# Kernel optimization log

Hardware: AMD Instinct MI355X
Metric: run time of the kernel (lower is better)

The kernel has to match this reference:

```python
import jax, jax.numpy as jnp
import numpy as np

N_HEADS = 16
ROPE_THETA = 10000.0


def _rotate_half(x):
    d = x.shape[-1] // 2
    return jnp.concatenate([-x[..., d:], x[..., :d]], axis=-1)


def setup_inputs() -> dict:
    key = jax.random.key(0)
    k1, k2, k3, k4 = jax.random.split(key, 4)
    B, S, D = 2, 2048, 2048
    std = 0.02
    return {
        "x": jax.random.normal(k1, (B, S, D), dtype=jnp.float32),
        "wq": std * jax.random.normal(k2, (D, D), dtype=jnp.float32),
        "wkv": std * jax.random.normal(k3, (D, 2 * D), dtype=jnp.float32),
        "wo": std * jax.random.normal(k4, (D, D), dtype=jnp.float32),
    }


def reference(x, wq, wkv, wo):
    # prefill case: kv_cache=None, past_length=0
    B, S, D = x.shape
    H = N_HEADS
    dh = D // H

    Q = x @ wq.T                                   # [B,S,D]
    K, V = jnp.split(x @ wkv, 2, axis=-1)          # [B,S,D] each

    q = Q.reshape(B, S, H, dh).transpose(0, 2, 1, 3)  # [B,H,S,dh]
    k = K.reshape(B, S, H, dh).transpose(0, 2, 1, 3)
    v = V.reshape(B, S, H, dh).transpose(0, 2, 1, 3)

    # RoPE tables (cos/sin of outer(pos, inv_freq), duplicated across halves)
    inv_freq = 1.0 / (ROPE_THETA ** (jnp.arange(0, dh, 2, dtype=jnp.float32) / dh))
    emb = jnp.arange(S, dtype=jnp.float32)[:, None] * inv_freq[None, :]  # [S, dh/2]
    cos = jnp.tile(jnp.cos(emb), (1, 2))[None, None]  # [1,1,S,dh]
    sin = jnp.tile(jnp.sin(emb), (1, 2))[None, None]

    q = q * cos + _rotate_half(q) * sin
    k = k * cos + _rotate_half(k) * sin

    scale = 1.0 / jnp.sqrt(jnp.asarray(dh, dtype=x.dtype))
    scores = jnp.einsum('bhqd,bhkd->bhqk', q, k) * scale  # [B,H,S,S]
    causal = jnp.tril(jnp.ones((S, S), dtype=bool))
    scores = jnp.where(causal[None, None], scores, -jnp.inf)
    attn = jax.nn.softmax(scores, axis=-1)

    out = jnp.einsum('bhqk,bhkd->bhqd', attn, v)          # [B,H,S,dh]
    out = out.transpose(0, 2, 1, 3).reshape(B, S, D)
    return out @ wo.T
```

## Files before the change

kernel.cpp:

```cpp
#include <hip/hip_runtime.h>
#include <stdint.h>

typedef unsigned short u16;
typedef __attribute__((ext_vector_type(8))) short short8;
typedef __attribute__((ext_vector_type(4))) float floatx4;

#define MFMA16(a, b, c) __builtin_amdgcn_mfma_f32_16x16x32_bf16(a, b, c, 0, 0, 0)

static __device__ __forceinline__ void gl_lds16(const void* g, void* l) {
  __builtin_amdgcn_global_load_lds(
      (const __attribute__((address_space(1))) uint32_t*)g,
      (__attribute__((address_space(3))) uint32_t*)l, 16, 0, 0);
}

static __device__ __forceinline__ float b2f(u16 u) {
  union { float f; unsigned u; } v;
  v.u = ((unsigned)u) << 16;
  return v.f;
}
static __device__ __forceinline__ u16 f2b(float f) {
  union { float f; unsigned u; } v;
  v.f = f;
  unsigned r = v.u + 0x7fffu + ((v.u >> 16) & 1u);
  return (u16)(r >> 16);
}
static __device__ __forceinline__ u16 f2b_rn(float f) {
  union { float f; unsigned u; } v;
  v.f = f;
  return (u16)((v.u + 0x8000u) >> 16);
}

static __device__ __forceinline__ int is_f32(const int* __restrict__ flag) {
  int s = 0;
#pragma unroll
  for (int i = 0; i < 32; ++i) s += flag[i];
  return s > 1000;
}

template <int CTRL>
static __device__ __forceinline__ float dppf(float x) {
  return __builtin_bit_cast(
      float, __builtin_amdgcn_update_dpp(0, __builtin_bit_cast(int, x), CTRL,
                                         0xF, 0xF, true));
}
static __device__ __forceinline__ float sum16(float x) {
  x += dppf<0x128>(x);
  x += dppf<0x124>(x);
  x += dppf<0x122>(x);
  x += dppf<0x121>(x);
  return x;
}
static __device__ __forceinline__ float max16(float x) {
  x = fmaxf(x, dppf<0x128>(x));
  x = fmaxf(x, dppf<0x124>(x));
  x = fmaxf(x, dppf<0x122>(x));
  x = fmaxf(x, dppf<0x121>(x));
  return x;
}

__global__ __launch_bounds__(256) void detect_f32(const u16* __restrict__ x,
                                                  int* __restrict__ flag) {
  __shared__ int cnt[256];
  int i = blockIdx.x * 256 + threadIdx.x;
  short8 v = ((const short8*)x)[i];
  int c = 0;
#pragma unroll
  for (int j = 0; j < 8; ++j) {
    int e = (((unsigned short)v[j]) >> 7) & 0xFF;
    c += (e >= 140) ? 1 : 0;
  }
  cnt[threadIdx.x] = c;
  __syncthreads();
  for (int s = 128; s > 0; s >>= 1) {
    if (threadIdx.x < (unsigned)s) cnt[threadIdx.x] += cnt[threadIdx.x + s];
    __syncthreads();
  }
  if (threadIdx.x == 0) flag[blockIdx.x] = cnt[0];
}

static __device__ __forceinline__ void conv8_body(const void* __restrict__ src,
                                                  u16* __restrict__ dst, int i,
                                                  int f32) {
  short8 r;
  if (f32) {
    const float4* s = (const float4*)src;
    float4 a = s[2 * i], b = s[2 * i + 1];
    r[0] = (short)f2b(a.x); r[1] = (short)f2b(a.y);
    r[2] = (short)f2b(a.z); r[3] = (short)f2b(a.w);
    r[4] = (short)f2b(b.x); r[5] = (short)f2b(b.y);
    r[6] = (short)f2b(b.z); r[7] = (short)f2b(b.w);
  } else {
    r = ((const short8*)src)[i];
  }
  ((short8*)dst)[i] = r;
}

__global__ __launch_bounds__(256) void convert_in8(const void* __restrict__ src,
                                                   u16* __restrict__ dst, int n8,
                                                   const int* __restrict__ flag) {
  int i = blockIdx.x * 256 + threadIdx.x;
  if (i >= n8) return;
  conv8_body(src, dst, i, is_f32(flag));
}

__global__ __launch_bounds__(256) void prep_fused(const void* __restrict__ x,
                                                  const void* __restrict__ wq,
                                                  const void* __restrict__ wkv,
                                                  u16* __restrict__ xb,
                                                  u16* __restrict__ wqb,
                                                  u16* __restrict__ wkvT,
                                                  const int* __restrict__ flag) {
  __shared__ u16 tile[32][33];
  int bid = blockIdx.x;
  int f = is_f32(flag);
  if (bid < 4096) {
    conv8_body(x, xb, bid * 256 + threadIdx.x, f);
  } else if (bid < 6144) {
    conv8_body(wq, wqb, (bid - 4096) * 256 + threadIdx.x, f);
  } else {
    int tb = bid - 6144;
    int c0 = (tb & 127) * 32, r0 = (tb >> 7) * 32;
    int lx = threadIdx.x & 31, ly = threadIdx.x >> 5;
#pragma unroll
    for (int i = 0; i < 32; i += 8) {
      size_t idx = (size_t)(r0 + ly + i) * 4096 + c0 + lx;
      tile[ly + i][lx] = f ? f2b(((const float*)wkv)[idx]) : ((const u16*)wkv)[idx];
    }
    __syncthreads();
#pragma unroll
    for (int i = 0; i < 32; i += 8)
      wkvT[(size_t)(c0 + ly + i) * 2048 + r0 + lx] = tile[lx][ly + i];
  }
}

__global__ __launch_bounds__(256) void mid_fused(u16* __restrict__ KV,
                                                 u16* __restrict__ Vt,
                                                 u16* __restrict__ Q) {
  __shared__ u16 tile[32][33];
  int bid = blockIdx.x;
  if (bid < 8192) {
    int b = bid >> 12;
    int d0 = (bid & 63) * 32, s0 = ((bid >> 6) & 63) * 32;
    int lx = threadIdx.x & 31, ly = threadIdx.x >> 5;
    const u16* src = KV + ((size_t)(b * 2048 + s0)) * 4096 + 2048 + d0;
#pragma unroll
    for (int i = 0; i < 32; i += 8)
      tile[ly + i][lx] = src[(size_t)(ly + i) * 4096 + lx];
    __syncthreads();
    u16* dst = Vt + ((size_t)(b * 2048 + d0)) * 2048 + s0;
#pragma unroll
    for (int i = 0; i < 32; i += 8)
      dst[(size_t)(ly + i) * 2048 + lx] = tile[lx][ly + i];
  } else {
    const float scale = 0.08838834764831845f;
    int idx = (bid - 8192) * 256 + threadIdx.x;
    int tok = idx >> 10;
    int rem = idx & 1023;
    int h = rem >> 6, i = rem & 63;
    int pos = tok & 2047;
    float f = __powf(10000.0f, -(float)(2 * i) * (1.0f / 128.0f));
    float ang = (float)pos * f;
    float s, c;
    sincosf(ang, &s, &c);

    size_t qb = (size_t)tok * 2048 + h * 128 + i;
    float q1 = b2f(Q[qb]), q2 = b2f(Q[qb + 64]);
    Q[qb] = f2b((q1 * c - q2 * s) * scale);
    Q[qb + 64] = f2b((q2 * c + q1 * s) * scale);

    size_t kb = (size_t)tok * 4096 + h * 128 + i;
    float k1 = b2f(KV[kb]), k2 = b2f(KV[kb + 64]);
    KV[kb] = f2b(k1 * c - k2 * s);
    KV[kb + 64] = f2b(k2 * c + k1 * s);
  }
}

__global__ __launch_bounds__(256) void gemm_nt(const u16* __restrict__ A,
                                               const u16* __restrict__ Bm,
                                               void* __restrict__ Cv,
                                               int M, int N, int K,
                                               const int* __restrict__ flag,
                                               int flag_mode) {
  __shared__ u16 Ash[128 * 64];
  __shared__ u16 Bsh[128 * 64];
  int tid = threadIdx.x, w = tid >> 6, lane = tid & 63;
  int quad = lane >> 4, l15 = lane & 15;
  int m0 = blockIdx.y * 128, n0 = blockIdx.x * 128;
  int wm = (w & 1) * 64, wn = (w >> 1) * 64;
  int f32out = flag_mode ? is_f32(flag) : 0;

  floatx4 acc[4][4];
#pragma unroll
  for (int i = 0; i < 4; ++i)
#pragma unroll
    for (int j = 0; j < 4; ++j) acc[i][j] = floatx4{0.f, 0.f, 0.f, 0.f};

  int srow = lane >> 3;
  int gch = (lane & 7) ^ srow;
  const u16* Ag = A + (size_t)(m0 + w * 32 + srow) * K + gch * 8;
  const u16* Bg = Bm + (size_t)(n0 + w * 32 + srow) * K + gch * 8;

  for (int k0 = 0; k0 < K; k0 += 64) {
    __syncthreads();
#pragma unroll
    for (int t = 0; t < 4; ++t) {
      gl_lds16(Ag + (size_t)t * 8 * K + k0, (void*)(Ash + (w * 32 + t * 8) * 64));
      gl_lds16(Bg + (size_t)t * 8 * K + k0, (void*)(Bsh + (w * 32 + t * 8) * 64));
    }
    __syncthreads();
#pragma unroll
    for (int kk = 0; kk < 2; ++kk) {
      int c = kk * 4 + quad;
      short8 af[4], bf[4];
#pragma unroll
      for (int i = 0; i < 4; ++i) {
        int m = wm + 16 * i + l15;
        af[i] = *(const short8*)(Ash + m * 64 + ((c ^ (m & 7)) << 3));
        int n = wn + 16 * i + l15;
        bf[i] = *(const short8*)(Bsh + n * 64 + ((c ^ (n & 7)) << 3));
      }
#pragma unroll
      for (int i = 0; i < 4; ++i)
#pragma unroll
        for (int j = 0; j < 4; ++j) acc[i][j] = MFMA16(af[i], bf[j], acc[i][j]);
    }
  }

#pragma unroll
  for (int i = 0; i < 4; ++i)
#pragma unroll
    for (int r = 0; r < 4; ++r) {
      int row = m0 + wm + 16 * i + quad * 4 + r;
      if (f32out) {
        float* cp = (float*)Cv + (size_t)row * N + n0 + wn + l15;
#pragma unroll
        for (int j = 0; j < 4; ++j) cp[16 * j] = acc[i][j][r];
      } else {
        u16* cp = (u16*)Cv + (size_t)row * N + n0 + wn + l15;
#pragma unroll
        for (int j = 0; j < 4; ++j) cp[16 * j] = f2b(acc[i][j][r]);
      }
    }
}

__global__ __launch_bounds__(512, 2) void gemm8(const u16* __restrict__ A,
                                                const u16* __restrict__ Bm,
                                                void* __restrict__ Cv,
                                                int M, int N, int K,
                                                const int* __restrict__ flag,
                                                int flag_mode) {
  __shared__ u16 Ash[2 * 256 * 64];
  __shared__ u16 Bsh[2 * 256 * 64];
  int tid = threadIdx.x, w = tid >> 6, lane = tid & 63;
  int quad = lane >> 4, l15 = lane & 15;
  int wr = w >> 2, wc = w & 3;
  int wm = wr * 128, wn = wc * 64;
  int m0 = blockIdx.y * 256, n0 = blockIdx.x * 256;
  int f32out = flag_mode ? is_f32(flag) : 0;
  const int NT = K >> 6;

  int srow8 = lane >> 3;
  int gch = (lane & 7) ^ srow8;
  const u16* Ag = A + (size_t)(m0 + w * 8 + srow8) * K + gch * 8;
  const u16* Bg = Bm + (size_t)(n0 + w * 8 + srow8) * K + gch * 8;
  int ldsrow = w * 8;

  floatx4 acc[8][4];
#pragma unroll
  for (int i = 0; i < 8; ++i)
#pragma unroll
    for (int j = 0; j < 4; ++j) acc[i][j] = floatx4{0.f, 0.f, 0.f, 0.f};

  int ch0 = ((quad ^ (l15 & 7)) << 3);
  int ch1 = (((4 + quad) ^ (l15 & 7)) << 3);

  auto stage = [&](int qi) {
    int tau = qi >> 2;
    int tc = tau < NT ? tau : NT - 1;
    int hh = qi & 3;
    int half = (hh & 1) * 128;
    int sbuf = (tau & 1) * (256 * 64);
    size_t kof = (size_t)tc * 64;
    if (hh < 2) {
      gl_lds16(Bg + (size_t)half * K + kof,
               (void*)(Bsh + sbuf + (half + ldsrow) * 64));
      gl_lds16(Bg + (size_t)(half + 64) * K + kof,
               (void*)(Bsh + sbuf + (half + 64 + ldsrow) * 64));
    } else {
      gl_lds16(Ag + (size_t)half * K + kof,
               (void*)(Ash + sbuf + (half + ldsrow) * 64));
      gl_lds16(Ag + (size_t)(half + 64) * K + kof,
               (void*)(Ash + sbuf + (half + 64 + ldsrow) * 64));
    }
  };

  stage(0); stage(1); stage(2); stage(3);
  __asm__ volatile("s_waitcnt vmcnt(4)" ::: "memory");
  stage(4); stage(5); stage(6);
  __asm__ volatile("s_waitcnt vmcnt(6)" ::: "memory");
  __builtin_amdgcn_s_barrier();

  for (int t = 0; t < NT; ++t) {
    u16* As = Ash + (t & 1) * (256 * 64);
    u16* Bs = Bsh + (t & 1) * (256 * 64);
    if (t) {
      __asm__ volatile("s_waitcnt vmcnt(6)" ::: "memory");
      __builtin_amdgcn_s_barrier();
    }
    int qb = 7 + 4 * t;
    short8 bf[8], af0[8], af1[8];

#pragma unroll
    for (int j = 0; j < 4; ++j) {
      int n = wn + 16 * j + l15;
      bf[2 * j] = *(const short8*)(Bs + n * 64 + ch0);
    }
#pragma unroll
    for (int i = 0; i < 4; ++i) {
      int m = wm + 16 * i + l15;
      af0[2 * i] = *(const short8*)(As + m * 64 + ch0);
    }
    stage(qb);
    __builtin_amdgcn_s_barrier();
    __asm__ volatile("s_waitcnt lgkmcnt(0)" ::: "memory");
    __builtin_amdgcn_sched_barrier(0);
    __builtin_amdgcn_s_setprio(1);
#pragma unroll
    for (int i = 0; i < 4; ++i)
#pragma unroll
      for (int j = 0; j < 4; ++j)
        acc[i][j] = MFMA16(af0[2 * i], bf[2 * j], acc[i][j]);
    __builtin_amdgcn_s_setprio(0);
    __builtin_amdgcn_s_barrier();

#pragma unroll
    for (int j = 0; j < 4; ++j) {
      int n = wn + 16 * j + l15;
      bf[2 * j + 1] = *(const short8*)(Bs + n * 64 + ch1);
    }
#pragma unroll
    for (int i = 0; i < 4; ++i) {
      int m = wm + 16 * i + l15;
      af0[2 * i + 1] = *(const short8*)(As + m * 64 + ch1);
    }
    stage(qb + 1);
    __builtin_amdgcn_s_barrier();
    __asm__ volatile("s_waitcnt lgkmcnt(0)" ::: "memory");
    __builtin_amdgcn_sched_barrier(0);
    __builtin_amdgcn_s_setprio(1);
#pragma unroll
    for (int i = 0; i < 4; ++i)
#pragma unroll
      for (int j = 0; j < 4; ++j)
        acc[i][j] = MFMA16(af0[2 * i + 1], bf[2 * j + 1], acc[i][j]);
    __builtin_amdgcn_s_setprio(0);
    __builtin_amdgcn_s_barrier();

#pragma unroll
    for (int i = 0; i < 4; ++i) {
      int m = wm + 64 + 16 * i + l15;
      af1[2 * i] = *(const short8*)(As + m * 64 + ch0);
    }
    stage(qb + 2);
    __builtin_amdgcn_s_barrier();
    __asm__ volatile("s_waitcnt lgkmcnt(0)" ::: "memory");
    __builtin_amdgcn_sched_barrier(0);
    __builtin_amdgcn_s_setprio(1);
#pragma unroll
    for (int i = 0; i < 4; ++i)
#pragma unroll
      for (int j = 0; j < 4; ++j)
        acc[4 + i][j] = MFMA16(af1[2 * i], bf[2 * j], acc[4 + i][j]);
    __builtin_amdgcn_s_setprio(0);
    __builtin_amdgcn_s_barrier();

#pragma unroll
    for (int i = 0; i < 4; ++i) {
      int m = wm + 64 + 16 * i + l15;
      af1[2 * i + 1] = *(const short8*)(As + m * 64 + ch1);
    }
    stage(qb + 3);
    __builtin_amdgcn_s_barrier();
    __asm__ volatile("s_waitcnt lgkmcnt(0)" ::: "memory");
    __builtin_amdgcn_sched_barrier(0);
    __builtin_amdgcn_s_setprio(1);
#pragma unroll
    for (int i = 0; i < 4; ++i)
#pragma unroll
      for (int j = 0; j < 4; ++j)
        acc[4 + i][j] = MFMA16(af1[2 * i + 1], bf[2 * j + 1], acc[4 + i][j]);
    __builtin_amdgcn_s_setprio(0);
    __builtin_amdgcn_s_barrier();
  }

#pragma unroll
  for (int i = 0; i < 8; ++i)
#pragma unroll
    for (int r = 0; r < 4; ++r) {
      int row = m0 + wm + 16 * i + quad * 4 + r;
      if (f32out) {
        float* cp = (float*)Cv + (size_t)row * N + n0 + wn + l15;
#pragma unroll
        for (int j = 0; j < 4; ++j) cp[16 * j] = acc[i][j][r];
      } else {
        u16* cp = (u16*)Cv + (size_t)row * N + n0 + wn + l15;
#pragma unroll
        for (int j = 0; j < 4; ++j) cp[16 * j] = f2b(acc[i][j][r]);
      }
    }
}

__global__ __launch_bounds__(512, 1) void flash_attn(const u16* __restrict__ Q,
                                                     const u16* __restrict__ KV,
                                                     const u16* __restrict__ Vt,
                                                     u16* __restrict__ O) {
  const int S = 2048, D = 2048, KVld = 4096;
  int bh = blockIdx.x;
  int qt = 15 - (int)blockIdx.y;
  int b = bh >> 4, h = bh & 15;
  int tid = threadIdx.x, w = tid >> 6, lane = tid & 63;
  int quad = lane >> 4, l15 = lane & 15;

  const u16* Qb = Q + (size_t)(b * S) * D + h * 128;
  const u16* Kb = KV + (size_t)(b * S) * KVld + h * 128;
  const u16* Vtb = Vt + ((size_t)(b * 2048 + h * 128)) * S;

  __shared__ u16 Ksh[128 * 128];
  __shared__ u16 Vsh[2][128 * 128];
  __shared__ u16 Psh[8][16 * 128];

  auto stage_k = [&](int kt) {
    int kb = kt * 128;
#pragma unroll
    for (int tt = 0; tt < 4; ++tt) {
      int r0 = w * 16 + tt * 4;
      int row = r0 + quad;
      int g = (l15 & 8) | ((l15 & 7) ^ (row & 7));
      gl_lds16(Kb + (size_t)(kb + row) * KVld + g * 8, (void*)(Ksh + r0 * 128));
    }
  };
  auto stage_v = [&](int kt, int buf) {
    int kb = kt * 128;
#pragma unroll
    for (int tt = 0; tt < 4; ++tt) {
      int d0 = w * 16 + tt * 4;
      int d = d0 + quad;
      int g = (l15 & 8) | ((l15 & 7) ^ (d & 7));
      gl_lds16(Vtb + (size_t)d * S + kb + g * 8, (void*)(Vsh[buf] + d0 * 128));
    }
  };

  int qw = qt * 128 + w * 16;

  short8 qf[4];
  {
    const u16* qp = Qb + (size_t)(qw + l15) * D + quad * 8;
#pragma unroll
    for (int kk = 0; kk < 4; ++kk) qf[kk] = *(const short8*)(qp + kk * 32);
  }

  floatx4 o[8];
#pragma unroll
  for (int t = 0; t < 8; ++t) o[t] = floatx4{0.f, 0.f, 0.f, 0.f};
  float mrow[4], lrow[4];
#pragma unroll
  for (int r = 0; r < 4; ++r) { mrow[r] = -1e30f; lrow[r] = 0.f; }

  int nk = qt + 1;
  stage_k(0);
  stage_v(0, 0);
  __syncthreads();

  for (int kt = 0; kt < nk; ++kt) {
    int kb = kt * 128;
    int cur = kt & 1;

    floatx4 sc[8];
#pragma unroll
    for (int nf = 0; nf < 8; ++nf) sc[nf] = floatx4{0.f, 0.f, 0.f, 0.f};
#pragma unroll
    for (int kk = 0; kk < 4; ++kk) {
      int c = kk * 4 + quad;
#pragma unroll
      for (int nf = 0; nf < 8; ++nf) {
        int n = nf * 16 + l15;
        int pc = (c & 8) | ((c & 7) ^ (n & 7));
        short8 kf = *(const short8*)(Ksh + n * 128 + pc * 8);
        sc[nf] = MFMA16(qf[kk], kf, sc[nf]);
      }
    }
    __syncthreads();
    if (kt + 1 < nk) {
      stage_k(kt + 1);
      stage_v(kt + 1, cur ^ 1);
    }

    bool masked = (kb + 127 > qw);
    floatx4 alv;
#pragma unroll
    for (int r = 0; r < 4; ++r) {
      int qg = qw + quad * 4 + r;
      float p[8];
#pragma unroll
      for (int g = 0; g < 8; ++g) {
        float vg = sc[g][r];
        if (masked) vg = (kb + 16 * g + l15 <= qg) ? vg : -1e30f;
        p[g] = vg;
      }
      float mx = fmaxf(fmaxf(fmaxf(p[0], p[1]), fmaxf(p[2], p[3])),
                       fmaxf(fmaxf(p[4], p[5]), fmaxf(p[6], p[7])));
      mx = max16(mx);
      float mn = fmaxf(mrow[r], mx);
      float al = __expf(mrow[r] - mn);
      mrow[r] = mn;
      float rs = 0.f;
#pragma unroll
      for (int g = 0; g < 8; ++g) {
        p[g] = __expf(p[g] - mn);
        rs += p[g];
      }
      rs = sum16(rs);
      lrow[r] = lrow[r] * al + rs;
      alv[r] = al;
      int m_ = quad * 4 + r;
      int sw = (m_ & 3) ^ ((m_ >> 2) << 1);
      int cb = l15 >> 3, e = l15 & 7;
      u16* pr = Psh[w] + m_ * 128;
#pragma unroll
      for (int g = 0; g < 8; ++g)
        pr[(((2 * g + cb) ^ sw) << 3) + e] = f2b_rn(p[g]);
    }
    if (__any((alv[0] != 1.f) || (alv[1] != 1.f) ||
              (alv[2] != 1.f) || (alv[3] != 1.f))) {
#pragma unroll
      for (int t = 0; t < 8; ++t) o[t] *= alv;
    }
    __asm__ volatile("s_waitcnt lgkmcnt(0)" ::: "memory");

    int psw = (l15 & 3) ^ ((l15 >> 2) << 1);
#pragma unroll
    for (int ks = 0; ks < 4; ++ks) {
      int c = ks * 4 + quad;
      short8 pf = *(const short8*)(Psh[w] + l15 * 128 + ((c ^ psw) << 3));
#pragma unroll
      for (int t = 0; t < 8; ++t) {
        int d = t * 16 + l15;
        int pc = (c & 8) | ((c & 7) ^ (d & 7));
        short8 vf = *(const short8*)(Vsh[cur] + d * 128 + pc * 8);
        o[t] = MFMA16(pf, vf, o[t]);
      }
    }
    __syncthreads();
  }

#pragma unroll
  for (int r = 0; r < 4; ++r) {
    float inv = 1.0f / lrow[r];
    int qg = qw + quad * 4 + r;
    u16* op = O + (size_t)(b * S + qg) * D + h * 128;
#pragma unroll
    for (int t = 0; t < 8; ++t) op[t * 16 + l15] = f2b(o[t][r] * inv);
  }
}

extern "C" void kernel_launch(void* const* d_in, const int* in_sizes, int n_in,
                              void* d_out, int out_size, void* d_ws, size_t ws_size,
                              hipStream_t stream) {
  const void* x = d_in[0];
  const void* wq = d_in[1];
  const void* wkv = d_in[2];
  const void* wo = d_in[3];

  int* flag = (int*)d_ws;
  u16* xb = (u16*)d_ws + 64;
  u16* Wbuf = xb + (size_t)8388608;
  u16* Qb = Wbuf + (size_t)8388608;
  u16* KVb = Qb + (size_t)8388608;
  u16* wqb = KVb + (size_t)8388608;
  u16* AO = xb;

  detect_f32<<<32, 256, 0, stream>>>((const u16*)x, flag);
  prep_fused<<<14336, 256, 0, stream>>>(x, wq, wkv, xb, wqb, Wbuf, flag);
  gemm_nt<<<dim3(16, 32), 256, 0, stream>>>(xb, wqb, Qb, 4096, 2048, 2048, flag, 0);
  gemm8<<<dim3(16, 16), 512, 0, stream>>>(xb, Wbuf, KVb, 4096, 4096, 2048, flag, 0);
  mid_fused<<<24576, 256, 0, stream>>>(KVb, Wbuf, Qb);
  flash_attn<<<dim3(32, 16), 512, 0, stream>>>(Qb, KVb, Wbuf, AO);
  convert_in8<<<2048, 256, 0, stream>>>(wo, Wbuf, 524288, flag);
  gemm_nt<<<dim3(16, 32), 256, 0, stream>>>(AO, Wbuf, d_out, 4096, 2048, 2048, flag, 1);
}
```

Measured before the change: 405.1 us.

## Fuse Q and KV projections into a single 256x256-tile GEMM launch

Replaces the separate Q projection GEMM (smaller-tile gemm_nt) and KV projection GEMM with one gemm8qkv launch whose grid spans both outputs, choosing the weight source and output buffer per block column. The converted wq is now staged in the output buffer instead of a separate workspace region. This removes one kernel launch and lets the Q projection use the larger, more heavily pipelined 8-wave tile. In exchange it adds a per-block branch and drops the f32-output path from this GEMM.

```diff
diff --git a/kernel.cpp b/kernel.cpp
--- a/kernel.cpp
+++ b/kernel.cpp
@@ -107,7 +107,7 @@
                                                   const void* __restrict__ wq,
                                                   const void* __restrict__ wkv,
                                                   u16* __restrict__ xb,
-                                                  u16* __restrict__ wqb,
+                                                  u16* __restrict__ wqd,
                                                   u16* __restrict__ wkvT,
                                                   const int* __restrict__ flag) {
   __shared__ u16 tile[32][33];
@@ -116,7 +116,7 @@
   if (bid < 4096) {
     conv8_body(x, xb, bid * 256 + threadIdx.x, f);
   } else if (bid < 6144) {
-    conv8_body(wq, wqb, (bid - 4096) * 256 + threadIdx.x, f);
+    conv8_body(wq, wqd, (bid - 4096) * 256 + threadIdx.x, f);
   } else {
     int tb = bid - 6144;
     int c0 = (tb & 127) * 32, r0 = (tb >> 7) * 32;
@@ -243,26 +243,35 @@
     }
 }
 
-__global__ __launch_bounds__(512, 2) void gemm8(const u16* __restrict__ A,
-                                                const u16* __restrict__ Bm,
-                                                void* __restrict__ Cv,
-                                                int M, int N, int K,
-                                                const int* __restrict__ flag,
-                                                int flag_mode) {
+__global__ __launch_bounds__(512, 2) void gemm8qkv(const u16* __restrict__ A,
+                                                   const u16* __restrict__ Bq,
+                                                   const u16* __restrict__ Bkv,
+                                                   u16* __restrict__ Cq,
+                                                   u16* __restrict__ Ckv) {
+  const int K = 2048;
+  const int NT = K >> 6;
   __shared__ u16 Ash[2 * 256 * 64];
   __shared__ u16 Bsh[2 * 256 * 64];
   int tid = threadIdx.x, w = tid >> 6, lane = tid & 63;
   int quad = lane >> 4, l15 = lane & 15;
   int wr = w >> 2, wc = w & 3;
   int wm = wr * 128, wn = wc * 64;
-  int m0 = blockIdx.y * 256, n0 = blockIdx.x * 256;
-  int f32out = flag_mode ? is_f32(flag) : 0;
-  const int NT = K >> 6;
+  int m0 = blockIdx.y * 256;
+  int n0g = blockIdx.x * 256;
+
+  const u16* Bsrc;
+  u16* Cd;
+  int ldc, ncol;
+  if (n0g < 2048) {
+    Bsrc = Bq; Cd = Cq; ldc = 2048; ncol = n0g;
+  } else {
+    Bsrc = Bkv; Cd = Ckv; ldc = 4096; ncol = n0g - 2048;
+  }
 
   int srow8 = lane >> 3;
   int gch = (lane & 7) ^ srow8;
   const u16* Ag = A + (size_t)(m0 + w * 8 + srow8) * K + gch * 8;
-  const u16* Bg = Bm + (size_t)(n0 + w * 8 + srow8) * K + gch * 8;
+  const u16* Bg = Bsrc + (size_t)(ncol + w * 8 + srow8) * K + gch * 8;
   int ldsrow = w * 8;
 
   floatx4 acc[8][4];
@@ -398,15 +407,9 @@
 #pragma unroll
     for (int r = 0; r < 4; ++r) {
       int row = m0 + wm + 16 * i + quad * 4 + r;
-      if (f32out) {
-        float* cp = (float*)Cv + (size_t)row * N + n0 + wn + l15;
-#pragma unroll
-        for (int j = 0; j < 4; ++j) cp[16 * j] = acc[i][j][r];
-      } else {
-        u16* cp = (u16*)Cv + (size_t)row * N + n0 + wn + l15;
-#pragma unroll
-        for (int j = 0; j < 4; ++j) cp[16 * j] = f2b(acc[i][j][r]);
-      }
+      u16* cp = Cd + (size_t)row * ldc + ncol + wn + l15;
+#pragma unroll
+      for (int j = 0; j < 4; ++j) cp[16 * j] = f2b(acc[i][j][r]);
     }
 }
 
@@ -576,13 +579,12 @@
   u16* Wbuf = xb + (size_t)8388608;
   u16* Qb = Wbuf + (size_t)8388608;
   u16* KVb = Qb + (size_t)8388608;
-  u16* wqb = KVb + (size_t)8388608;
+  u16* wqd = (u16*)d_out;
   u16* AO = xb;
 
   detect_f32<<<32, 256, 0, stream>>>((const u16*)x, flag);
-  prep_fused<<<14336, 256, 0, stream>>>(x, wq, wkv, xb, wqb, Wbuf, flag);
-  gemm_nt<<<dim3(16, 32), 256, 0, stream>>>(xb, wqb, Qb, 4096, 2048, 2048, flag, 0);
-  gemm8<<<dim3(16, 16), 512, 0, stream>>>(xb, Wbuf, KVb, 4096, 4096, 2048, flag, 0);
+  prep_fused<<<14336, 256, 0, stream>>>(x, wq, wkv, xb, wqd, Wbuf, flag);
+  gemm8qkv<<<dim3(24, 16), 512, 0, stream>>>(xb, wqd, Wbuf, Qb, KVb);
   mid_fused<<<24576, 256, 0, stream>>>(KVb, Wbuf, Qb);
   flash_attn<<<dim3(32, 16), 512, 0, stream>>>(Qb, KVb, Wbuf, AO);
   convert_in8<<<2048, 256, 0, stream>>>(wo, Wbuf, 524288, flag);
```

Measured after the change: 419.1 us. 1.03x slower.
